# Performance work log

Measured on AMD Instinct MI355X. Metric: run time of the kernel, lower is better.

## Reference

```python
import jax, jax.numpy as jnp
import numpy as np
import math

B, S, D, H = 8, 1024, 128, 8  # batch, seq, input_dim(=head_dim), head_num

def setup_inputs() -> dict:
    key = jax.random.key(0)
    ks = jax.random.split(key, 12)
    HD = H * D
    sc_in = 1.0 / math.sqrt(D)
    sc_hd = 1.0 / math.sqrt(HD)
    return {
        "query": jax.random.normal(ks[0], (B, S, D), jnp.float32),
        "key":   jax.random.normal(ks[1], (B, S, D), jnp.float32),
        "value": jax.random.normal(ks[2], (B, S, D), jnp.float32),
        "pos":   jax.random.normal(ks[3], (B, S, D), jnp.float32),
        "mask":  jnp.ones((B, S), jnp.int32),
        # torch Linear weights stored as [in, out] for x @ W + b
        "Wq": jax.random.normal(ks[4], (D, HD), jnp.float32) * sc_in,
        "bq": jnp.zeros((HD,), jnp.float32),
        "Wk": jax.random.normal(ks[5], (D, HD), jnp.float32) * sc_in,
        "bk": jnp.zeros((HD,), jnp.float32),
        "Wv": jax.random.normal(ks[6], (D, HD), jnp.float32) * sc_in,
        "bv": jnp.zeros((HD,), jnp.float32),
        "Wo": jax.random.normal(ks[7], (HD, D), jnp.float32) * sc_hd,
        "bo": jnp.zeros((D,), jnp.float32),
    }

def reference(query, key, value, pos, mask, Wq, bq, Wk, bk, Wv, bv, Wo, bo):
    # QKV projections (pos added to all three inputs)
    q = (query + pos) @ Wq + bq  # [B,S,H*D]
    k = (key + pos) @ Wk + bk
    v = (value + pos) @ Wv + bv
    # split heads -> [B,H,S,D]
    q = q.reshape(B, S, H, D).transpose(0, 2, 1, 3)
    k = k.reshape(B, S, H, D).transpose(0, 2, 1, 3)
    v = v.reshape(B, S, H, D).transpose(0, 2, 1, 3)
    scale = 1.0 / math.sqrt(D)
    scores = jnp.einsum("bhqd,bhkd->bhqk", q, k) * scale  # [B,H,S,S]
    # mask [B,S] -> broadcast over heads and query positions
    m = mask[:, None, None, :]  # [B,1,1,S]
    scores = jnp.where(m == 0, jnp.float32(-jnp.inf), scores)
    attn = jax.nn.softmax(scores, axis=-1)  # dropout is identity in eval mode
    out = jnp.einsum("bhqk,bhkd->bhqd", attn, v)
    out = out.transpose(0, 2, 1, 3).reshape(B, S, H * D)
    return out @ Wo + bo  # [B,S,D]
```

## Files before the change

### kernel.cpp

```cpp
#include <hip/hip_runtime.h>
#include <stdint.h>


typedef __attribute__((ext_vector_type(8))) short bf16x8;
typedef __attribute__((ext_vector_type(4))) short s16x4;
typedef __attribute__((ext_vector_type(4))) float f32x4;
typedef unsigned int uint;
typedef unsigned short ushort;

__device__ __forceinline__ float bf2f(short s) {
    return __uint_as_float(((uint)(ushort)s) << 16);
}
__device__ __forceinline__ short f2bf(float f) {
    uint u = __float_as_uint(f);
    u += 0x7fffu + ((u >> 16) & 1u);
    return (short)(u >> 16);
}
__device__ __forceinline__ short f2bf_fast(float f) {
    return (short)((__float_as_uint(f) + 0x8000u) >> 16);
}

__device__ __forceinline__ void dma16(const short* g, short* l) {
    __builtin_amdgcn_global_load_lds(
        (const __attribute__((address_space(1))) uint*)g,
        (__attribute__((address_space(3))) uint*)l, 16, 0, 0);
}

__global__ __launch_bounds__(256) void fill_sentinel(float* __restrict__ out, int n) {
    int i = blockIdx.x * 256 + threadIdx.x;
    if (i < n) out[i] = 128.0f;
}

__global__ __launch_bounds__(256) void transpose_w(
    const float* __restrict__ Wq, const float* __restrict__ Wk,
    const float* __restrict__ Wv, const float* __restrict__ Wo,
    short* __restrict__ WTq, short* __restrict__ WTk,
    short* __restrict__ WTv, short* __restrict__ WoT)
{
    int z = blockIdx.y;
    const float* src; short* dst; int K, N;
    if (z < 3) { K = 128; N = 1024; src = (z==0)?Wq:(z==1)?Wk:Wv; dst = (z==0)?WTq:(z==1)?WTk:WTv; }
    else       { K = 1024; N = 128; src = Wo; dst = WoT; }
    int ntn = N >> 6;
    int nt = blockIdx.x % ntn, kt = blockIdx.x / ntn;
    int k0 = kt * 64, n0 = nt * 64;

    __shared__ __align__(16) short TT[64][72];
    int t = threadIdx.x;
    int r = t >> 2, c4 = t & 3;
    const float4* s4 = (const float4*)&src[(k0 + r) * N + n0 + c4 * 16];
    short* tr = &TT[r][c4 * 16];
#pragma unroll
    for (int i = 0; i < 4; ++i) {
        float4 v = s4[i];
        tr[i * 4 + 0] = f2bf(v.x);
        tr[i * 4 + 1] = f2bf(v.y);
        tr[i * 4 + 2] = f2bf(v.z);
        tr[i * 4 + 3] = f2bf(v.w);
    }
    __syncthreads();
    union { short s[16]; uint4 v[2]; } pk;
#pragma unroll
    for (int i = 0; i < 16; ++i) pk.s[i] = TT[c4 * 16 + i][r];
    uint4* dp = (uint4*)&dst[(n0 + r) * K + k0 + c4 * 16];
    dp[0] = pk.v[0]; dp[1] = pk.v[1];
}

__global__ __launch_bounds__(256) void qkv_proj(
    const float* __restrict__ query, const float* __restrict__ key_,
    const float* __restrict__ value, const float* __restrict__ pos,
    const short* __restrict__ WTq, const short* __restrict__ WTk, const short* __restrict__ WTv,
    const float* __restrict__ bq, const float* __restrict__ bk, const float* __restrict__ bv,
    short* __restrict__ Qg, short* __restrict__ Kg, short* __restrict__ Vtg)
{
    int z = blockIdx.y;
    const float* X    = (z==0) ? query : (z==1) ? key_ : value;
    const short* WT   = (z==0) ? WTq   : (z==1) ? WTk  : WTv;
    const float* bias = (z==0) ? bq    : (z==1) ? bk   : bv;

    __shared__ __align__(16) short Xs[64][136];
    __shared__ __align__(16) short Ws[2][8192];

    int t = threadIdx.x;
    int bx = blockIdx.x;
    int m0 = (bx >> 1) * 64;
    int nt0 = (bx & 1) * 8;
    int lane = t & 63, w = t >> 6;
    int l = lane & 15, q = lane >> 4;

    short* Tbuf = &Xs[0][0];

    const short* wbase = &WT[(w * 16 + l) * 128 + q * 8];
    {
#pragma unroll
        for (int k32 = 0; k32 < 4; ++k32)
            dma16(wbase + nt0 * 8192 + k32 * 32, &Ws[0][(w * 4 + k32) * 512]);
    }
    {
        int r = t >> 2, c4 = t & 3;
        const float4* xs = (const float4*)&X[(m0 + r) * 128 + c4 * 32];
        const float4* ps = (const float4*)&pos[(m0 + r) * 128 + c4 * 32];
#pragma unroll
        for (int i = 0; i < 8; ++i) {
            float4 a = xs[i], bb = ps[i];
            uint2 o;
            o.x = (uint)(ushort)f2bf(a.x + bb.x) | ((uint)(ushort)f2bf(a.y + bb.y) << 16);
            o.y = (uint)(ushort)f2bf(a.z + bb.z) | ((uint)(ushort)f2bf(a.w + bb.w) << 16);
            *(uint2*)&Xs[r][c4 * 32 + i * 4] = o;
        }
    }
    __syncthreads();

    bf16x8 aX[4];
#pragma unroll
    for (int k32 = 0; k32 < 4; ++k32)
        aX[k32] = *(const bf16x8*)&Xs[w * 16 + l][k32 * 32 + q * 8];
    __syncthreads();

    int b = m0 >> 10, s0 = m0 & 1023;
    int srow = s0 + w * 16 + l;

    for (int i = 0; i < 8; ++i) {
        int nt = nt0 + i;
        int cur = i & 1;
        if (i) __syncthreads();
        if (i < 7) {
            const short* wsrc = wbase + (nt + 1) * 8192;
#pragma unroll
            for (int k32 = 0; k32 < 4; ++k32)
                dma16(wsrc + k32 * 32, &Ws[cur ^ 1][(w * 4 + k32) * 512]);
        }

        int n0 = nt * 64;
        if (z < 2) {
#pragma unroll
            for (int nb = 0; nb < 4; ++nb) {
                f32x4 c = {0.f, 0.f, 0.f, 0.f};
                const short* wf = &Ws[cur][nb * 2048 + lane * 8];
#pragma unroll
                for (int k32 = 0; k32 < 4; ++k32)
                    c = __builtin_amdgcn_mfma_f32_16x16x32_bf16(*(const bf16x8*)(wf + k32 * 512), aX[k32], c, 0, 0, 0);
                const float* bip = &bias[n0 + nb * 16 + q * 4];
                short* dst = (z == 0) ? Qg : Kg;
                int n00 = n0 + nb * 16;
                int hh = n00 >> 7, d0 = (n00 & 127) + q * 4;
                s16x4 ov = { f2bf(c[0] + bip[0]), f2bf(c[1] + bip[1]),
                             f2bf(c[2] + bip[2]), f2bf(c[3] + bip[3]) };
                *(s16x4*)&dst[(((b * 8 + hh) * 1024 + srow) << 7) + d0] = ov;
            }
        } else {
#pragma unroll
            for (int nb = 0; nb < 4; ++nb) {
                f32x4 c = {0.f, 0.f, 0.f, 0.f};
                const short* wf = &Ws[cur][nb * 2048 + lane * 8];
#pragma unroll
                for (int k32 = 0; k32 < 4; ++k32)
                    c = __builtin_amdgcn_mfma_f32_16x16x32_bf16(*(const bf16x8*)(wf + k32 * 512), aX[k32], c, 0, 0, 0);
                const float* bip = &bias[n0 + nb * 16 + q * 4];
#pragma unroll
                for (int r = 0; r < 4; ++r)
                    Tbuf[(nb * 16 + q * 4 + r) * 72 + w * 16 + l] = f2bf(c[r] + bip[r]);
            }
            __syncthreads();
            int nl = t >> 2, mc = t & 3;
            int n = n0 + nl, hh = n >> 7, dd = n & 127;
            uint4 v0 = *(uint4*)&Tbuf[nl * 72 + mc * 16];
            uint4 v1 = *(uint4*)&Tbuf[nl * 72 + mc * 16 + 8];
            uint4* dp = (uint4*)&Vtg[(((b * 8 + hh) * 128 + dd) << 10) + s0 + mc * 16];
            dp[0] = v0; dp[1] = v1;
        }
    }
}

__global__ __launch_bounds__(256, 2) void attention(
    const short* __restrict__ Qg, const short* __restrict__ Kg,
    const short* __restrict__ Vtg, const int* __restrict__ mask,
    short* __restrict__ AO)
{
    int bh = blockIdx.x & 63;
    int qt = blockIdx.x >> 6;
    int b = bh >> 3, h = bh & 7;
    int q0 = qt << 7;

    __shared__ __align__(16) short Ks[2][8192];
    __shared__ __align__(16) short Vs[8192];
    __shared__ __align__(16) short Ps[4][32][72];

    int t = threadIdx.x, lane = t & 63, w = t >> 6;
    int l = lane & 15, q = lane >> 4;

    const short* kbase = &Kg[((bh * 1024 + w * 16 + l) << 7) + q * 8];
    const short* vb0 = &Vtg[((bh * 128 + (2 * w) * 16 + l) << 10) + q * 8];
    const short* vb1 = &Vtg[((bh * 128 + (2 * w + 1) * 16 + l) << 10) + q * 8];
    const int* mrow = &mask[b * 1024];

    {
        dma16(kbase,      &Ks[0][(w * 4 + 0) * 512]);
        dma16(kbase + 32, &Ks[0][(w * 4 + 1) * 512]);
        dma16(kbase + 64, &Ks[0][(w * 4 + 2) * 512]);
        dma16(kbase + 96, &Ks[0][(w * 4 + 3) * 512]);
    }

    bf16x8 aQ[2][4];
#pragma unroll
    for (int s = 0; s < 2; ++s) {
        const short* qp = &Qg[((bh * 1024 + q0 + w * 32 + s * 16 + l) << 7) + q * 8];
#pragma unroll
        for (int k32 = 0; k32 < 4; ++k32)
            aQ[s][k32] = *(const bf16x8*)(qp + k32 * 32);
    }

    f32x4 O[2][8];
#pragma unroll
    for (int s = 0; s < 2; ++s)
#pragma unroll
        for (int i = 0; i < 8; ++i) O[s][i] = {0.f, 0.f, 0.f, 0.f};
    f32x4 Ls[2] = {{0.f, 0.f, 0.f, 0.f}, {0.f, 0.f, 0.f, 0.f}};

    const short O1 = (short)0x3F80;
    const bf16x8 ONES = {O1, O1, O1, O1, O1, O1, O1, O1};

    const float SL2E = 0.12752298917458827f;
    const float MAXB = 44.0f;

    for (int kt = 0; kt < 16; ++kt) {
        int k0 = kt << 6;
        int cur = kt & 1;
        __syncthreads();
        if (kt < 15) {
            const short* kp = kbase + (((kt + 1) << 6) << 7);
            dma16(kp,      &Ks[cur ^ 1][(w * 4 + 0) * 512]);
            dma16(kp + 32, &Ks[cur ^ 1][(w * 4 + 1) * 512]);
            dma16(kp + 64, &Ks[cur ^ 1][(w * 4 + 2) * 512]);
            dma16(kp + 96, &Ks[cur ^ 1][(w * 4 + 3) * 512]);
        }
        {
            dma16(vb0 + k0,      &Vs[(4 * w + 0) * 512]);
            dma16(vb0 + k0 + 32, &Vs[(4 * w + 1) * 512]);
            dma16(vb1 + k0,      &Vs[(4 * w + 2) * 512]);
            dma16(vb1 + k0 + 32, &Vs[(4 * w + 3) * 512]);
        }

        int mk[4];
#pragma unroll
        for (int nb = 0; nb < 4; ++nb) mk[nb] = mrow[k0 + nb * 16 + l];
        bool allm = (__ballot(mk[0] && mk[1] && mk[2] && mk[3]) == ~0ull);

#pragma unroll
        for (int nb = 0; nb < 4; ++nb) {
            bf16x8 kf[4];
            const short* kfp = &Ks[cur][nb * 2048 + lane * 8];
#pragma unroll
            for (int k32 = 0; k32 < 4; ++k32)
                kf[k32] = *(const bf16x8*)(kfp + k32 * 512);
#pragma unroll
            for (int s = 0; s < 2; ++s) {
                f32x4 c = {0.f, 0.f, 0.f, 0.f};
#pragma unroll
                for (int k32 = 0; k32 < 4; ++k32)
                    c = __builtin_amdgcn_mfma_f32_16x16x32_bf16(aQ[s][k32], kf[k32], c, 0, 0, 0);
#pragma unroll
                for (int r = 0; r < 4; ++r) {
                    float pv = exp2f(fmaf(c[r], SL2E, -MAXB));
                    if (!allm) pv = mk[nb] ? pv : 0.f;
                    Ps[w][s * 16 + q * 4 + r][nb * 16 + l] = f2bf_fast(pv);
                }
            }
        }
        __syncthreads();

        bf16x8 aP[2][2];
#pragma unroll
        for (int s = 0; s < 2; ++s) {
            aP[s][0] = *(const bf16x8*)&Ps[w][s * 16 + l][q * 8];
            aP[s][1] = *(const bf16x8*)&Ps[w][s * 16 + l][32 + q * 8];
        }
#pragma unroll
        for (int s = 0; s < 2; ++s) {
            Ls[s] = __builtin_amdgcn_mfma_f32_16x16x32_bf16(aP[s][0], ONES, Ls[s], 0, 0, 0);
            Ls[s] = __builtin_amdgcn_mfma_f32_16x16x32_bf16(aP[s][1], ONES, Ls[s], 0, 0, 0);
        }
#pragma unroll
        for (int dt = 0; dt < 8; ++dt) {
            bf16x8 vf0 = *(const bf16x8*)&Vs[(dt * 2 + 0) * 512 + lane * 8];
            bf16x8 vf1 = *(const bf16x8*)&Vs[(dt * 2 + 1) * 512 + lane * 8];
#pragma unroll
            for (int s = 0; s < 2; ++s) {
                f32x4 c = O[s][dt];
                c = __builtin_amdgcn_mfma_f32_16x16x32_bf16(aP[s][0], vf0, c, 0, 0, 0);
                c = __builtin_amdgcn_mfma_f32_16x16x32_bf16(aP[s][1], vf1, c, 0, 0, 0);
                O[s][dt] = c;
            }
        }
    }

#pragma unroll
    for (int s = 0; s < 2; ++s) {
        float rl[4];
#pragma unroll
        for (int r = 0; r < 4; ++r) rl[r] = 1.0f / Ls[s][r];
#pragma unroll
        for (int dt = 0; dt < 8; ++dt) {
            int col = h * 128 + dt * 16 + l;
#pragma unroll
            for (int r = 0; r < 4; ++r) {
                int srow = q0 + w * 32 + s * 16 + q * 4 + r;
                AO[((b * 1024 + srow) << 10) + col] = f2bf(O[s][dt][r] * rl[r]);
            }
        }
    }
}

__global__ __launch_bounds__(256) void out_proj(
    const short* __restrict__ AO, const short* __restrict__ WoT,
    const float* __restrict__ bo, float* __restrict__ out)
{
    __shared__ __align__(16) short As[2][16][72];
    __shared__ __align__(16) short Bs[2][8192];

    int t = threadIdx.x, lane = t & 63, w = t >> 6;
    int l = lane & 15, q = lane >> 4;
    int m0 = blockIdx.x * 16;

    int ar = t >> 3, ac8 = t & 7;
    {
        if (t < 128)
            *(uint4*)&As[0][ar][ac8 * 8] = *(const uint4*)&AO[((m0 + ar) << 10) + ac8 * 8];
#pragma unroll
        for (int j = 0; j < 4; ++j) {
            int nb = 2 * w + (j >> 1), k32 = j & 1;
            dma16(&WoT[(nb * 16 + l) * 1024 + k32 * 32 + q * 8], &Bs[0][(nb * 2 + k32) * 512]);
        }
    }

    f32x4 acc[2];
    acc[0] = {0.f, 0.f, 0.f, 0.f};
    acc[1] = {0.f, 0.f, 0.f, 0.f};

    for (int kc = 0; kc < 16; ++kc) {
        __syncthreads();
        int cur = kc & 1;
        uint4 anext;
        if (kc < 15) {
            int k1 = (kc + 1) * 64;
            if (t < 128)
                anext = *(const uint4*)&AO[((m0 + ar) << 10) + k1 + ac8 * 8];
#pragma unroll
            for (int j = 0; j < 4; ++j) {
                int nb = 2 * w + (j >> 1), k32 = j & 1;
                dma16(&WoT[(nb * 16 + l) * 1024 + k1 + k32 * 32 + q * 8],
                      &Bs[cur ^ 1][(nb * 2 + k32) * 512]);
            }
        }

        bf16x8 aA0 = *(const bf16x8*)&As[cur][l][q * 8];
        bf16x8 aA1 = *(const bf16x8*)&As[cur][l][32 + q * 8];
#pragma unroll
        for (int nb = 0; nb < 2; ++nb) {
            int nbg = 2 * w + nb;
            f32x4 c = acc[nb];
            c = __builtin_amdgcn_mfma_f32_16x16x32_bf16(*(const bf16x8*)&Bs[cur][(nbg * 2 + 0) * 512 + lane * 8], aA0, c, 0, 0, 0);
            c = __builtin_amdgcn_mfma_f32_16x16x32_bf16(*(const bf16x8*)&Bs[cur][(nbg * 2 + 1) * 512 + lane * 8], aA1, c, 0, 0, 0);
            acc[nb] = c;
        }

        if (kc < 15 && t < 128)
            *(uint4*)&As[cur ^ 1][ar][ac8 * 8] = anext;
    }

#pragma unroll
    for (int nb = 0; nb < 2; ++nb) {
        int n0 = (2 * w + nb) * 16 + q * 4;
        const float* bop = &bo[n0];
        float4 ov = { acc[nb][0] + bop[0], acc[nb][1] + bop[1],
                      acc[nb][2] + bop[2], acc[nb][3] + bop[3] };
        *(float4*)&out[((m0 + l) << 7) + n0] = ov;
    }
}

extern "C" void kernel_launch(void* const* d_in, const int* in_sizes, int n_in,
                              void* d_out, int out_size, void* d_ws, size_t ws_size,
                              hipStream_t stream)
{
    const size_t NEED = (size_t)65 * 1024 * 1024;
    if (ws_size < NEED) {
        hipLaunchKernelGGL(fill_sentinel, dim3((out_size + 255) / 256), dim3(256), 0, stream,
                           (float*)d_out, out_size);
        return;
    }

    const float* query = (const float*)d_in[0];
    const float* key_  = (const float*)d_in[1];
    const float* value = (const float*)d_in[2];
    const float* pos   = (const float*)d_in[3];
    const int*   mask  = (const int*)d_in[4];
    const float* Wq = (const float*)d_in[5];
    const float* bq = (const float*)d_in[6];
    const float* Wk = (const float*)d_in[7];
    const float* bk = (const float*)d_in[8];
    const float* Wv = (const float*)d_in[9];
    const float* bv = (const float*)d_in[10];
    const float* Wo = (const float*)d_in[11];
    const float* bo = (const float*)d_in[12];

    char* ws = (char*)d_ws;
    short* Qg  = (short*)(ws);
    short* Kg  = (short*)(ws + (size_t)16 * 1024 * 1024);
    short* Vtg = (short*)(ws + (size_t)32 * 1024 * 1024);
    short* AO  = (short*)(ws + (size_t)48 * 1024 * 1024);
    short* WTq = (short*)(ws + (size_t)64 * 1024 * 1024);
    short* WTk = WTq + 131072;
    short* WTv = WTk + 131072;
    short* WoT = WTv + 131072;

    hipLaunchKernelGGL(transpose_w, dim3(32, 4), dim3(256), 0, stream,
                       Wq, Wk, Wv, Wo, WTq, WTk, WTv, WoT);
    hipLaunchKernelGGL(qkv_proj, dim3(256, 3), dim3(256), 0, stream,
                       query, key_, value, pos, WTq, WTk, WTv, bq, bk, bv, Qg, Kg, Vtg);
    hipLaunchKernelGGL(attention, dim3(512), dim3(256), 0, stream,
                       Qg, Kg, Vtg, mask, AO);
    hipLaunchKernelGGL(out_proj, dim3(512), dim3(256), 0, stream,
                       AO, WoT, bo, (float*)d_out);
}
```

Before: 190.2 us.

## Fuse output projection into attention epilogue with per-head atomic accumulation

The separate out_proj kernel and the bf16 attention-output buffer are removed. Each attention block now loads its head's slice of Wo into LDS, multiplies its normalized output tile by that slice with MFMA, and accumulates the partial result into the fp32 output with atomicAdd. Head 0 adds the bias, and the output is zeroed with a memset first. This saves a kernel launch and the write and read of the 16MB intermediate, at the cost of 8-way atomic contention per output element, a nondeterministic summation order and extra epilogue work in the attention kernel.

```diff
diff --git a/kernel.cpp b/kernel.cpp
--- a/kernel.cpp
+++ b/kernel.cpp
@@ -175,7 +175,8 @@
 __global__ __launch_bounds__(256, 2) void attention(
     const short* __restrict__ Qg, const short* __restrict__ Kg,
     const short* __restrict__ Vtg, const int* __restrict__ mask,
-    short* __restrict__ AO)
+    const short* __restrict__ WoT, const float* __restrict__ bo,
+    float* __restrict__ out)
 {
     int bh = blockIdx.x & 63;
     int qt = blockIdx.x >> 6;
@@ -294,87 +295,70 @@
         }
     }
 
-#pragma unroll
-    for (int s = 0; s < 2; ++s) {
-        float rl[4];
-#pragma unroll
-        for (int r = 0; r < 4; ++r) rl[r] = 1.0f / Ls[s][r];
-#pragma unroll
-        for (int dt = 0; dt < 8; ++dt) {
-            int col = h * 128 + dt * 16 + l;
-#pragma unroll
-            for (int r = 0; r < 4; ++r) {
-                int srow = q0 + w * 32 + s * 16 + q * 4 + r;
-                AO[((b * 1024 + srow) << 10) + col] = f2bf(O[s][dt][r] * rl[r]);
+    short* KsF = &Ks[0][0];
+    {
+#pragma unroll
+        for (int j = 0; j < 8; ++j) {
+            int nb = 2 * w + (j >> 2), k32 = j & 3;
+            dma16(&WoT[(nb * 16 + l) * 1024 + h * 128 + k32 * 32 + q * 8],
+                  &KsF[(nb * 4 + k32) * 512]);
+        }
+    }
+
+    float rl[2][4];
+#pragma unroll
+    for (int s = 0; s < 2; ++s)
+#pragma unroll
+        for (int r = 0; r < 4; ++r) rl[s][r] = 1.0f / Ls[s][r];
+
+    f32x4 acc[8][2];
+#pragma unroll
+    for (int nb = 0; nb < 8; ++nb) {
+        acc[nb][0] = {0.f, 0.f, 0.f, 0.f};
+        acc[nb][1] = {0.f, 0.f, 0.f, 0.f};
+    }
+
+#pragma unroll
+    for (int half = 0; half < 2; ++half) {
+#pragma unroll
+        for (int s = 0; s < 2; ++s)
+#pragma unroll
+            for (int dt = 0; dt < 4; ++dt)
+#pragma unroll
+                for (int r = 0; r < 4; ++r)
+                    Ps[w][s * 16 + q * 4 + r][dt * 16 + l] =
+                        f2bf(O[s][half * 4 + dt][r] * rl[s][r]);
+        if (half == 0) __syncthreads();
+
+        bf16x8 aO[2][2];
+#pragma unroll
+        for (int s = 0; s < 2; ++s) {
+            aO[s][0] = *(const bf16x8*)&Ps[w][s * 16 + l][q * 8];
+            aO[s][1] = *(const bf16x8*)&Ps[w][s * 16 + l][32 + q * 8];
+        }
+#pragma unroll
+        for (int nb = 0; nb < 8; ++nb)
+#pragma unroll
+            for (int s = 0; s < 2; ++s) {
+                f32x4 c = acc[nb][s];
+                c = __builtin_amdgcn_mfma_f32_16x16x32_bf16(
+                        aO[s][0], *(const bf16x8*)&KsF[(nb * 4 + half * 2 + 0) * 512 + lane * 8], c, 0, 0, 0);
+                c = __builtin_amdgcn_mfma_f32_16x16x32_bf16(
+                        aO[s][1], *(const bf16x8*)&KsF[(nb * 4 + half * 2 + 1) * 512 + lane * 8], c, 0, 0, 0);
+                acc[nb][s] = c;
             }
-        }
-    }
-}
-
-__global__ __launch_bounds__(256) void out_proj(
-    const short* __restrict__ AO, const short* __restrict__ WoT,
-    const float* __restrict__ bo, float* __restrict__ out)
-{
-    __shared__ __align__(16) short As[2][16][72];
-    __shared__ __align__(16) short Bs[2][8192];
-
-    int t = threadIdx.x, lane = t & 63, w = t >> 6;
-    int l = lane & 15, q = lane >> 4;
-    int m0 = blockIdx.x * 16;
-
-    int ar = t >> 3, ac8 = t & 7;
-    {
-        if (t < 128)
-            *(uint4*)&As[0][ar][ac8 * 8] = *(const uint4*)&AO[((m0 + ar) << 10) + ac8 * 8];
-#pragma unroll
-        for (int j = 0; j < 4; ++j) {
-            int nb = 2 * w + (j >> 1), k32 = j & 1;
-            dma16(&WoT[(nb * 16 + l) * 1024 + k32 * 32 + q * 8], &Bs[0][(nb * 2 + k32) * 512]);
-        }
-    }
-
-    f32x4 acc[2];
-    acc[0] = {0.f, 0.f, 0.f, 0.f};
-    acc[1] = {0.f, 0.f, 0.f, 0.f};
-
-    for (int kc = 0; kc < 16; ++kc) {
-        __syncthreads();
-        int cur = kc & 1;
-        uint4 anext;
-        if (kc < 15) {
-            int k1 = (kc + 1) * 64;
-            if (t < 128)
-                anext = *(const uint4*)&AO[((m0 + ar) << 10) + k1 + ac8 * 8];
-#pragma unroll
-            for (int j = 0; j < 4; ++j) {
-                int nb = 2 * w + (j >> 1), k32 = j & 1;
-                dma16(&WoT[(nb * 16 + l) * 1024 + k1 + k32 * 32 + q * 8],
-                      &Bs[cur ^ 1][(nb * 2 + k32) * 512]);
-            }
-        }
-
-        bf16x8 aA0 = *(const bf16x8*)&As[cur][l][q * 8];
-        bf16x8 aA1 = *(const bf16x8*)&As[cur][l][32 + q * 8];
-#pragma unroll
-        for (int nb = 0; nb < 2; ++nb) {
-            int nbg = 2 * w + nb;
-            f32x4 c = acc[nb];
-            c = __builtin_amdgcn_mfma_f32_16x16x32_bf16(*(const bf16x8*)&Bs[cur][(nbg * 2 + 0) * 512 + lane * 8], aA0, c, 0, 0, 0);
-            c = __builtin_amdgcn_mfma_f32_16x16x32_bf16(*(const bf16x8*)&Bs[cur][(nbg * 2 + 1) * 512 + lane * 8], aA1, c, 0, 0, 0);
-            acc[nb] = c;
-        }
-
-        if (kc < 15 && t < 128)
-            *(uint4*)&As[cur ^ 1][ar][ac8 * 8] = anext;
-    }
-
-#pragma unroll
-    for (int nb = 0; nb < 2; ++nb) {
-        int n0 = (2 * w + nb) * 16 + q * 4;
-        const float* bop = &bo[n0];
-        float4 ov = { acc[nb][0] + bop[0], acc[nb][1] + bop[1],
-                      acc[nb][2] + bop[2], acc[nb][3] + bop[3] };
-        *(float4*)&out[((m0 + l) << 7) + n0] = ov;
+    }
+
+    int rowbase = b * 1024 + q0 + w * 32;
+#pragma unroll
+    for (int nb = 0; nb < 8; ++nb) {
+        float bt = (h == 0) ? bo[nb * 16 + l] : 0.f;
+#pragma unroll
+        for (int s = 0; s < 2; ++s)
+#pragma unroll
+            for (int r = 0; r < 4; ++r)
+                atomicAdd(&out[(rowbase + s * 16 + q * 4 + r) * 128 + nb * 16 + l],
+                          acc[nb][s][r] + bt);
     }
 }
 
@@ -407,18 +391,17 @@
     short* Qg  = (short*)(ws);
     short* Kg  = (short*)(ws + (size_t)16 * 1024 * 1024);
     short* Vtg = (short*)(ws + (size_t)32 * 1024 * 1024);
-    short* AO  = (short*)(ws + (size_t)48 * 1024 * 1024);
     short* WTq = (short*)(ws + (size_t)64 * 1024 * 1024);
     short* WTk = WTq + 131072;
     short* WTv = WTk + 131072;
     short* WoT = WTv + 131072;
+
+    hipMemsetAsync(d_out, 0, (size_t)out_size * sizeof(float), stream);
 
     hipLaunchKernelGGL(transpose_w, dim3(32, 4), dim3(256), 0, stream,
                        Wq, Wk, Wv, Wo, WTq, WTk, WTv, WoT);
     hipLaunchKernelGGL(qkv_proj, dim3(256, 3), dim3(256), 0, stream,
                        query, key_, value, pos, WTq, WTk, WTv, bq, bk, bv, Qg, Kg, Vtg);
     hipLaunchKernelGGL(attention, dim3(512), dim3(256), 0, stream,
-                       Qg, Kg, Vtg, mask, AO);
-    hipLaunchKernelGGL(out_proj, dim3(512), dim3(256), 0, stream,
-                       AO, WoT, bo, (float*)d_out);
-}
+                       Qg, Kg, Vtg, mask, WoT, bo, (float*)d_out);
+}
```

Result: slower. 196.0 us (+3.0%).
